# Kernel tuning notes

Hardware: AMD Instinct MI355X
Metric: run time of the kernel (lower is better)

Reference implementation:

```python
import jax, jax.numpy as jnp
import numpy as np

TEMPERATURE = 0.2
HYPER_GAMMA = 0.5
EPS = 1e-12  # torch F.normalize / cosine_similarity eps guard (1e-12 / 1e-8)

def setup_inputs() -> dict:
    key = jax.random.key(0)
    k1, k2 = jax.random.split(key)
    B, D = 4096, 1024
    return {
        "emb_i": jax.random.normal(k1, (B, D), dtype=jnp.float32),
        "emb_j": jax.random.normal(k2, (B, D), dtype=jnp.float32),
    }

def _l2_normalize(x, eps=EPS):
    n = jnp.sqrt(jnp.sum(x * x, axis=1, keepdims=True))
    return x / jnp.maximum(n, eps)

def reference(emb_i, emb_j):
    B = emb_i.shape[0]
    z_i = _l2_normalize(emb_i)
    z_j = _l2_normalize(emb_j)
    # cosine similarity of unit vectors == dot product; sim[a, b] = <z_j[a], z_i[b]>
    sim = jnp.einsum('ad,bd->ab', z_j, z_i)  # [B, B]
    sim_positive = jnp.diagonal(sim)
    positives_exp = jnp.exp(-sim_positive + TEMPERATURE)
    neg_mask = 1.0 - jnp.eye(B, dtype=sim.dtype)
    negatives_exp = neg_mask * jnp.exp(sim - TEMPERATURE)
    positives_sum = jnp.sum(jnp.log1p(positives_exp)) / B
    negatives_sum = jnp.sum(jnp.log1p(negatives_exp)) / (B * (B - 1))
    return HYPER_GAMMA * positives_sum + (1.0 - HYPER_GAMMA) * negatives_sum
```

## Files before the change

### kernel.cpp

```cpp
#include <hip/hip_runtime.h>
#include <math.h>

#define B_ROWS 4096
#define D_DIM  1024
static constexpr float TEMP = 0.2f;
static constexpr float FP8_SCALE = 16.0f;
static constexpr float INV_S2 = 1.0f / 256.0f;

typedef __attribute__((ext_vector_type(4)))  int   i32x4;
typedef __attribute__((ext_vector_type(8)))  int   i32x8;
typedef __attribute__((ext_vector_type(4)))  float f32x4;

__device__ inline void gload_lds16(const unsigned char* g, unsigned char* l) {
    __builtin_amdgcn_global_load_lds(
        (const __attribute__((address_space(1))) unsigned int*)g,
        (__attribute__((address_space(3))) unsigned int*)l,
        16, 0, 0);
}

__device__ inline i32x8 read_frag(const unsigned char* p, int o0, int o1) {
    i32x4 lo = *(const i32x4*)(p + o0);
    i32x4 hi = *(const i32x4*)(p + o1);
    return __builtin_shufflevector(lo, hi, 0, 1, 2, 3, 4, 5, 6, 7);
}

#define MX_MFMA(A, Bv, C) __builtin_amdgcn_mfma_scale_f32_16x16x128_f8f6f4( \
    (A), (Bv), (C), 0, 0, 0, 0x7f7f7f7f, 0, 0x7f7f7f7f)

__device__ inline unsigned int cvt4_fp8(float4 v) {
    int d = 0;
    d = __builtin_amdgcn_cvt_pk_fp8_f32(v.x, v.y, d, false);
    d = __builtin_amdgcn_cvt_pk_fp8_f32(v.z, v.w, d, true);
    return (unsigned int)d;
}


__global__ __launch_bounds__(256) void norm_cast_kernel(
        const float* __restrict__ emb_i, const float* __restrict__ emb_j,
        unsigned char* __restrict__ Zi8, unsigned char* __restrict__ Zj8,
        float* __restrict__ w) {
    const int tid = threadIdx.x;
    if (blockIdx.x == 0 && tid == 0) {
        w[0] = 0.0f; w[1] = 0.0f;
        ((unsigned int*)w)[2] = 0u;
    }
    const int wave = tid >> 6, lane = tid & 63;
    const int row = blockIdx.x * 4 + wave;
    const float* src; unsigned char* dst; int r;
    if (row < B_ROWS) { src = emb_i; dst = Zi8; r = row; }
    else              { src = emb_j; dst = Zj8; r = row - B_ROWS; }

    const float4* p = (const float4*)(src + (size_t)r * D_DIM) + 4 * lane;
    float4 v0 = p[0], v1 = p[1], v2 = p[2], v3 = p[3];
    float s = v0.x*v0.x + v0.y*v0.y + v0.z*v0.z + v0.w*v0.w
            + v1.x*v1.x + v1.y*v1.y + v1.z*v1.z + v1.w*v1.w
            + v2.x*v2.x + v2.y*v2.y + v2.z*v2.z + v2.w*v2.w
            + v3.x*v3.x + v3.y*v3.y + v3.z*v3.z + v3.w*v3.w;
    #pragma unroll
    for (int m = 1; m < 64; m <<= 1) s += __shfl_xor(s, m, 64);
    const float inv = FP8_SCALE / fmaxf(sqrtf(s), 1e-12f);

    float4 a0 = {v0.x*inv, v0.y*inv, v0.z*inv, v0.w*inv};
    float4 a1 = {v1.x*inv, v1.y*inv, v1.z*inv, v1.w*inv};
    float4 a2 = {v2.x*inv, v2.y*inv, v2.z*inv, v2.w*inv};
    float4 a3 = {v3.x*inv, v3.y*inv, v3.z*inv, v3.w*inv};
    i32x4 o = { (int)cvt4_fp8(a0), (int)cvt4_fp8(a1),
                (int)cvt4_fp8(a2), (int)cvt4_fp8(a3) };
    ((i32x4*)(dst + (size_t)r * D_DIM))[lane] = o;
}

__global__ __launch_bounds__(256) void simloss_mfma_mxfp8_kernel(
        const unsigned char* __restrict__ Zi8,
        const unsigned char* __restrict__ Zj8,
        float* __restrict__ w, float* __restrict__ out) {
    __shared__ __align__(16) unsigned char lA[128 * 128];
    __shared__ __align__(16) unsigned char lB[128 * 128];
    __shared__ float rn[4], rp[4];

    const int tid  = threadIdx.x;
    const int lane = tid & 63;
    const int wave = tid >> 6;
    const int wy = wave >> 1, wx = wave & 1;

    const int bid = blockIdx.x;
    const int xcd = bid & 7;
    const int loc = bid >> 3;
    const int by  = ((xcd >> 2) << 4) + (loc >> 3);
    const int bx  = ((xcd & 3) << 3) + (loc & 7);
    const int rowBase = by * 128;
    const int colBase = bx * 128;

    const int srow = lane >> 3;
    const int sc   = (lane & 7) ^ srow;
    const unsigned char* gA = Zj8 + (size_t)(rowBase + 32*wave + srow) * D_DIM + sc*16;
    const unsigned char* gB = Zi8 + (size_t)(colBase + 32*wave + srow) * D_DIM + sc*16;
    unsigned char* sA = lA + wave * 4096;
    unsigned char* sB = lB + wave * 4096;

    const int lr16 = lane & 15;
    const int g    = lane >> 4;
    const int o0 = ((((g << 1) + 0) ^ (lane & 7)) << 4);
    const int o1 = ((((g << 1) + 1) ^ (lane & 7)) << 4);
    const unsigned char* fA = lA + (wy * 64 + lr16) * 128;
    const unsigned char* fB = lB + (wx * 64 + lr16) * 128;

    f32x4 acc[4][4];
    #pragma unroll
    for (int i = 0; i < 4; ++i)
        #pragma unroll
        for (int j = 0; j < 4; ++j)
            acc[i][j] = (f32x4){0.f, 0.f, 0.f, 0.f};

    for (int it = 0; it < 8; ++it) {
        __syncthreads();
        const int k0 = it * 128;
        #pragma unroll
        for (int n = 0; n < 4; ++n) {
            gload_lds16(gA + (size_t)(n*8) * D_DIM + k0, sA + n*1024);
            gload_lds16(gB + (size_t)(n*8) * D_DIM + k0, sB + n*1024);
        }
        __syncthreads();

        i32x8 a0 = read_frag(fA,        o0, o1);
        i32x8 a1 = read_frag(fA + 2048, o0, o1);
        i32x8 a2 = read_frag(fA + 4096, o0, o1);
        i32x8 a3 = read_frag(fA + 6144, o0, o1);
        i32x8 b0 = read_frag(fB,        o0, o1);
        i32x8 b1 = read_frag(fB + 2048, o0, o1);
        i32x8 b2 = read_frag(fB + 4096, o0, o1);
        i32x8 b3 = read_frag(fB + 6144, o0, o1);
        acc[0][0] = MX_MFMA(a0, b0, acc[0][0]);
        acc[0][1] = MX_MFMA(a0, b1, acc[0][1]);
        acc[0][2] = MX_MFMA(a0, b2, acc[0][2]);
        acc[0][3] = MX_MFMA(a0, b3, acc[0][3]);
        acc[1][0] = MX_MFMA(a1, b0, acc[1][0]);
        acc[1][1] = MX_MFMA(a1, b1, acc[1][1]);
        acc[1][2] = MX_MFMA(a1, b2, acc[1][2]);
        acc[1][3] = MX_MFMA(a1, b3, acc[1][3]);
        acc[2][0] = MX_MFMA(a2, b0, acc[2][0]);
        acc[2][1] = MX_MFMA(a2, b1, acc[2][1]);
        acc[2][2] = MX_MFMA(a2, b2, acc[2][2]);
        acc[2][3] = MX_MFMA(a2, b3, acc[2][3]);
        acc[3][0] = MX_MFMA(a3, b0, acc[3][0]);
        acc[3][1] = MX_MFMA(a3, b1, acc[3][1]);
        acc[3][2] = MX_MFMA(a3, b2, acc[3][2]);
        acc[3][3] = MX_MFMA(a3, b3, acc[3][3]);
    }

    float neg = 0.f, pos = 0.f;
    const int bc = colBase + wx * 64 + lr16;
    #pragma unroll
    for (int i = 0; i < 4; ++i) {
        const int abase = rowBase + wy * 64 + i * 16 + g * 4;
        #pragma unroll
        for (int j = 0; j < 4; ++j) {
            const int b = bc + j * 16;
            #pragma unroll
            for (int r = 0; r < 4; ++r) {
                const float x = acc[i][j][r] * INV_S2 - TEMP;
                if (abase + r == b) pos += __logf(1.0f + __expf(-x));
                else                neg += __logf(1.0f + __expf(x));
            }
        }
    }
    #pragma unroll
    for (int o = 32; o > 0; o >>= 1) {
        neg += __shfl_down(neg, o, 64);
        pos += __shfl_down(pos, o, 64);
    }
    if (lane == 0) { rn[wave] = neg; rp[wave] = pos; }
    __syncthreads();
    if (tid == 0) {
        atomicAdd(&w[1], rn[0] + rn[1] + rn[2] + rn[3]);
        if (bx == by)
            atomicAdd(&w[0], rp[0] + rp[1] + rp[2] + rp[3]);
        __threadfence();
        unsigned int done = atomicAdd(((unsigned int*)w) + 2, 1u);
        if (done == gridDim.x - 1) {
            const float psum = atomicAdd(&w[0], 0.0f);
            const float nsum = atomicAdd(&w[1], 0.0f);
            out[0] = 0.5f * (psum / (float)B_ROWS)
                   + 0.5f * (nsum / ((float)B_ROWS * (float)(B_ROWS - 1)));
        }
    }
}

extern "C" void kernel_launch(void* const* d_in, const int* in_sizes, int n_in,
                              void* d_out, int out_size, void* d_ws, size_t ws_size,
                              hipStream_t stream) {
    const float* emb_i = (const float*)d_in[0];
    const float* emb_j = (const float*)d_in[1];
    float* w = (float*)d_ws;
    unsigned char* Zi8 = (unsigned char*)(w + 16);
    unsigned char* Zj8 = Zi8 + (size_t)B_ROWS * D_DIM;
    float* out = (float*)d_out;

    norm_cast_kernel<<<2 * B_ROWS / 4, 256, 0, stream>>>(emb_i, emb_j, Zi8, Zj8, w);
    simloss_mfma_mxfp8_kernel<<<1024, 256, 0, stream>>>(Zi8, Zj8, w, out);
}
```

Measured before the change: 126.2 us.

## Double-buffer LDS tiles and use eight waves per block in MXFP8 GEMM

The similarity GEMM kernel now runs 8 waves per 128x128 tile, each computing a 64x32 sub-tile, and double-buffers the LDS staging so the next K-slice's global-to-LDS loads are issued before the current slice's MFMAs. One barrier per iteration replaces two. MFMA blocks are wrapped in s_setprio to favour matrix issue. The intent is to hide global load latency and raise occupancy, at the cost of doubling LDS per block to 64KB and reloading A fragments in more waves.

```diff
diff --git a/kernel.cpp b/kernel.cpp
--- a/kernel.cpp
+++ b/kernel.cpp
@@ -69,18 +69,17 @@
     ((i32x4*)(dst + (size_t)r * D_DIM))[lane] = o;
 }
 
-__global__ __launch_bounds__(256) void simloss_mfma_mxfp8_kernel(
+__global__ __launch_bounds__(512, 4) void simloss_mfma_mxfp8_kernel(
         const unsigned char* __restrict__ Zi8,
         const unsigned char* __restrict__ Zj8,
         float* __restrict__ w, float* __restrict__ out) {
-    __shared__ __align__(16) unsigned char lA[128 * 128];
-    __shared__ __align__(16) unsigned char lB[128 * 128];
-    __shared__ float rn[4], rp[4];
+    __shared__ __align__(16) unsigned char lds[2 * 32768];
+    __shared__ float rn[8], rp[8];
 
     const int tid  = threadIdx.x;
     const int lane = tid & 63;
     const int wave = tid >> 6;
-    const int wy = wave >> 1, wx = wave & 1;
+    const int wy = wave >> 2, wx = wave & 3;
 
     const int bid = blockIdx.x;
     const int xcd = bid & 7;
@@ -92,68 +91,72 @@
 
     const int srow = lane >> 3;
     const int sc   = (lane & 7) ^ srow;
-    const unsigned char* gA = Zj8 + (size_t)(rowBase + 32*wave + srow) * D_DIM + sc*16;
-    const unsigned char* gB = Zi8 + (size_t)(colBase + 32*wave + srow) * D_DIM + sc*16;
-    unsigned char* sA = lA + wave * 4096;
-    unsigned char* sB = lB + wave * 4096;
+    const unsigned char* gA = Zj8 + (size_t)(rowBase + 16*wave + srow) * D_DIM + sc*16;
+    const unsigned char* gB = Zi8 + (size_t)(colBase + 16*wave + srow) * D_DIM + sc*16;
+    const int sAoff = wave * 2048;
+    const int sBoff = 16384 + wave * 2048;
+
+#define STAGE(k0, bo) do {                                                     \
+        _Pragma("unroll")                                                      \
+        for (int n = 0; n < 2; ++n) {                                          \
+            gload_lds16(gA + (size_t)(n*8) * D_DIM + (k0),                     \
+                        lds + (bo) + sAoff + n*1024);                          \
+            gload_lds16(gB + (size_t)(n*8) * D_DIM + (k0),                     \
+                        lds + (bo) + sBoff + n*1024);                          \
+        }                                                                      \
+    } while (0)
 
     const int lr16 = lane & 15;
     const int g    = lane >> 4;
     const int o0 = ((((g << 1) + 0) ^ (lane & 7)) << 4);
     const int o1 = ((((g << 1) + 1) ^ (lane & 7)) << 4);
-    const unsigned char* fA = lA + (wy * 64 + lr16) * 128;
-    const unsigned char* fB = lB + (wx * 64 + lr16) * 128;
-
-    f32x4 acc[4][4];
+    const int fAoff = (wy * 64 + lr16) * 128;
+    const int fBoff = 16384 + (wx * 32 + lr16) * 128;
+
+    f32x4 acc[4][2];
     #pragma unroll
     for (int i = 0; i < 4; ++i)
         #pragma unroll
-        for (int j = 0; j < 4; ++j)
+        for (int j = 0; j < 2; ++j)
             acc[i][j] = (f32x4){0.f, 0.f, 0.f, 0.f};
 
+    STAGE(0, 0);
+    __syncthreads();
+    int cur = 0;
     for (int it = 0; it < 8; ++it) {
-        __syncthreads();
-        const int k0 = it * 128;
-        #pragma unroll
-        for (int n = 0; n < 4; ++n) {
-            gload_lds16(gA + (size_t)(n*8) * D_DIM + k0, sA + n*1024);
-            gload_lds16(gB + (size_t)(n*8) * D_DIM + k0, sB + n*1024);
-        }
-        __syncthreads();
-
+        if (it < 7) STAGE((it + 1) * 128, cur ^ 32768);
+
+        const unsigned char* fA = lds + cur + fAoff;
+        const unsigned char* fB = lds + cur + fBoff;
         i32x8 a0 = read_frag(fA,        o0, o1);
         i32x8 a1 = read_frag(fA + 2048, o0, o1);
         i32x8 a2 = read_frag(fA + 4096, o0, o1);
         i32x8 a3 = read_frag(fA + 6144, o0, o1);
         i32x8 b0 = read_frag(fB,        o0, o1);
         i32x8 b1 = read_frag(fB + 2048, o0, o1);
-        i32x8 b2 = read_frag(fB + 4096, o0, o1);
-        i32x8 b3 = read_frag(fB + 6144, o0, o1);
+        __builtin_amdgcn_s_setprio(1);
         acc[0][0] = MX_MFMA(a0, b0, acc[0][0]);
         acc[0][1] = MX_MFMA(a0, b1, acc[0][1]);
-        acc[0][2] = MX_MFMA(a0, b2, acc[0][2]);
-        acc[0][3] = MX_MFMA(a0, b3, acc[0][3]);
         acc[1][0] = MX_MFMA(a1, b0, acc[1][0]);
         acc[1][1] = MX_MFMA(a1, b1, acc[1][1]);
-        acc[1][2] = MX_MFMA(a1, b2, acc[1][2]);
-        acc[1][3] = MX_MFMA(a1, b3, acc[1][3]);
         acc[2][0] = MX_MFMA(a2, b0, acc[2][0]);
         acc[2][1] = MX_MFMA(a2, b1, acc[2][1]);
-        acc[2][2] = MX_MFMA(a2, b2, acc[2][2]);
-        acc[2][3] = MX_MFMA(a2, b3, acc[2][3]);
         acc[3][0] = MX_MFMA(a3, b0, acc[3][0]);
         acc[3][1] = MX_MFMA(a3, b1, acc[3][1]);
-        acc[3][2] = MX_MFMA(a3, b2, acc[3][2]);
-        acc[3][3] = MX_MFMA(a3, b3, acc[3][3]);
-    }
+        __builtin_amdgcn_s_setprio(0);
+
+        __syncthreads();
+        cur ^= 32768;
+    }
+#undef STAGE
 
     float neg = 0.f, pos = 0.f;
-    const int bc = colBase + wx * 64 + lr16;
+    const int bc = colBase + wx * 32 + lr16;
     #pragma unroll
     for (int i = 0; i < 4; ++i) {
         const int abase = rowBase + wy * 64 + i * 16 + g * 4;
         #pragma unroll
-        for (int j = 0; j < 4; ++j) {
+        for (int j = 0; j < 2; ++j) {
             const int b = bc + j * 16;
             #pragma unroll
             for (int r = 0; r < 4; ++r) {
@@ -171,9 +174,11 @@
     if (lane == 0) { rn[wave] = neg; rp[wave] = pos; }
     __syncthreads();
     if (tid == 0) {
-        atomicAdd(&w[1], rn[0] + rn[1] + rn[2] + rn[3]);
-        if (bx == by)
-            atomicAdd(&w[0], rp[0] + rp[1] + rp[2] + rp[3]);
+        float n8 = 0.f, p8 = 0.f;
+        #pragma unroll
+        for (int k = 0; k < 8; ++k) { n8 += rn[k]; p8 += rp[k]; }
+        atomicAdd(&w[1], n8);
+        if (bx == by) atomicAdd(&w[0], p8);
         __threadfence();
         unsigned int done = atomicAdd(((unsigned int*)w) + 2, 1u);
         if (done == gridDim.x - 1) {
@@ -196,5 +201,5 @@
     float* out = (float*)d_out;
 
     norm_cast_kernel<<<2 * B_ROWS / 4, 256, 0, stream>>>(emb_i, emb_j, Zi8, Zj8, w);
-    simloss_mfma_mxfp8_kernel<<<1024, 256, 0, stream>>>(Zi8, Zj8, w, out);
-}
+    simloss_mfma_mxfp8_kernel<<<1024, 512, 0, stream>>>(Zi8, Zj8, w, out);
+}
```

After: 453.1 us. 259% more time.
